# Kernel optimization log

Measured on AMD Instinct MI355X. Metric: run time of the kernel, lower is better.

The kernel has to match this reference:

```python
import jax, jax.numpy as jnp
import numpy as np

B, C, N_MAX = 32, 1, 1024
HID, CLS, ATT_E, ATT_H = 128, 64, 64, 128
D = HID + CLS            # node_state_dim = hidden + class_repr
EDGE_F = 2 * ATT_E       # 128
K_MIX = 20
N_GNN = B * C * N_MAX    # 32768 GNN nodes
N_FEAT = N_GNN + 1       # node_feat rows after zero-pad row
E = 200_000
E_OUT = 500_000
NUM_SUB = 1024
NUM_PROP = 2             # num_GNN_prop (num_GNN_layers = 1)


def _lin(k, din, dout):
    k1, k2 = jax.random.split(k)
    s = 1.0 / np.sqrt(din)
    return (jax.random.uniform(k1, (din, dout), minval=-s, maxval=s),
            jax.random.uniform(k2, (dout,), minval=-s, maxval=s))


def setup_inputs() -> dict:
    key = jax.random.key(0)
    ks = jax.random.split(key, 30)
    inp = {}
    inp['A_pad'] = (jax.random.uniform(ks[0], (B, C, N_MAX, N_MAX)) < 0.05).astype(jnp.float32)
    inp['edges'] = jax.random.randint(ks[1], (E, 2), 0, N_GNN)
    inp['att_idx'] = jax.random.randint(ks[2], (N_GNN,), 0, ATT_E)
    inp['node_idx_feat'] = jax.random.randint(ks[3], (N_GNN,), 0, N_FEAT)
    inp['class_label'] = jax.random.randint(ks[4], (N_GNN,), 0, 2)
    inp['node_idx_gnn'] = jax.random.randint(ks[5], (E_OUT, 2), 0, N_GNN)
    inp['label'] = (jax.random.uniform(ks[6], (E_OUT,)) < 0.3).astype(jnp.float32)
    inp['subgraph_idx'] = jax.random.randint(ks[7], (E_OUT,), 0, NUM_SUB)
    # learned parameters
    inp['W_dec'], inp['b_dec'] = _lin(ks[8], N_MAX, HID)
    inp['class_emb'] = jax.random.normal(ks[9], (2, CLS)) * 0.1
    inp['W_msg1'], inp['b_msg1'] = _lin(ks[10], D + EDGE_F, D)
    inp['W_msg2'], inp['b_msg2'] = _lin(ks[11], D, D)
    inp['W_att1'], inp['b_att1'] = _lin(ks[12], D + EDGE_F, ATT_H)
    inp['W_att2'], inp['b_att2'] = _lin(ks[13], ATT_H, D)
    inp['W_ih'], inp['b_ih'] = _lin(ks[14], D, 3 * D)
    inp['W_hh'], inp['b_hh'] = _lin(ks[15], D, 3 * D)
    inp['Wt1'], inp['bt1'] = _lin(ks[16], D, HID)
    inp['Wt2'], inp['bt2'] = _lin(ks[17], HID, HID)
    inp['Wt3'], inp['bt3'] = _lin(ks[18], HID, K_MIX)
    inp['Wa1'], inp['ba1'] = _lin(ks[19], D, HID)
    inp['Wa2'], inp['ba2'] = _lin(ks[20], HID, HID)
    inp['Wa3'], inp['ba3'] = _lin(ks[21], HID, K_MIX)
    return inp


def _gran_forward(A_pad, label, W_dec, b_dec, class_emb,
                  W_msg1, b_msg1, W_msg2, b_msg2, W_att1, b_att1, W_att2, b_att2,
                  W_ih, b_ih, W_hh, b_hh, Wt1, bt1, Wt2, bt2, Wt3, bt3,
                  Wa1, ba1, Wa2, ba2, Wa3, ba3,
                  edges, att_idx, node_idx_feat, class_label, node_idx_gnn, subgraph_idx):
    # decoder_input: (B*C*N_max, N_max) -> hidden, then zero-pad one row on top
    A = A_pad.reshape(B * C * N_MAX, N_MAX)
    node_feat = A @ W_dec + b_dec                                   # [N_GNN, HID]
    node_feat = jnp.concatenate([jnp.zeros((1, HID), node_feat.dtype), node_feat], axis=0)
    # att_edge_feat: one-hot(att_idx[src]) || one-hot(att_idx[dst])  (scatter of ones)
    att_edge_feat = jnp.concatenate([
        jax.nn.one_hot(att_idx[edges[:, 0]], ATT_E, dtype=node_feat.dtype),
        jax.nn.one_hot(att_idx[edges[:, 1]], ATT_E, dtype=node_feat.dtype)], axis=1)  # [E, 128]
    # node state = gathered feat ++ class representation
    state = jnp.concatenate([node_feat[node_idx_feat], class_emb[class_label]], axis=1)  # [N_GNN, D]

    src, dst = edges[:, 0], edges[:, 1]

    def prop(state):
        diff = state[src] - state[dst]                              # gather node-diff [E, D]
        ei = jnp.concatenate([diff, att_edge_feat], axis=1)          # [E, D+128]
        msg = jax.nn.relu(ei @ W_msg1 + b_msg1) @ W_msg2 + b_msg2   # edge MLP [E, D]
        att = jax.nn.sigmoid(jax.nn.relu(ei @ W_att1 + b_att1) @ W_att2 + b_att2)
        agg = jax.ops.segment_sum(msg * att, dst, num_segments=N_GNN)  # scatter-add [N_GNN, D]
        # GRUCell(agg, state)
        gi = agg @ W_ih + b_ih
        gh = state @ W_hh + b_hh
        ir, iz, inn = jnp.split(gi, 3, axis=1)
        hr, hz, hn = jnp.split(gh, 3, axis=1)
        r = jax.nn.sigmoid(ir + hr)
        z = jax.nn.sigmoid(iz + hz)
        n = jnp.tanh(inn + r * hn)
        return (1.0 - z) * n + z * state

    for _ in range(NUM_PROP):
        state = prop(state)

    # output edge predictions from state diffs
    dout = state[node_idx_gnn[:, 0]] - state[node_idx_gnn[:, 1]]    # [E_OUT, D]
    h = jax.nn.relu(jax.nn.relu(dout @ Wt1 + bt1) @ Wt2 + bt2)
    log_theta = h @ Wt3 + bt3                                        # [E_OUT, K]
    g = jax.nn.relu(jax.nn.relu(dout @ Wa1 + ba1) @ Wa2 + ba2)
    log_alpha = jax.nn.log_softmax(g @ Wa3 + ba3, axis=1)            # [E_OUT, K]

    # mixture Bernoulli loss (BCEWithLogits, pos_weight=1): softplus(x) - x*y
    adj_loss = jax.nn.softplus(log_theta) - log_theta * label[:, None]
    const = jax.ops.segment_sum(jnp.ones((E_OUT,), log_theta.dtype), subgraph_idx, num_segments=NUM_SUB)
    const = jnp.maximum(const, 1.0)  # guard empty subgraphs with random indices
    red_loss = jax.ops.segment_sum(adj_loss, subgraph_idx, num_segments=NUM_SUB)
    red_alpha = jax.ops.segment_sum(log_alpha, subgraph_idx, num_segments=NUM_SUB) / const[:, None]
    log_prob = jax.nn.logsumexp(-red_loss + red_alpha, axis=1)       # [NUM_SUB]
    return -jnp.sum(log_prob) / float(E_OUT)


def reference(A_pad, edges, att_idx, node_idx_feat, class_label, node_idx_gnn, label, subgraph_idx,
              W_dec, b_dec, class_emb, W_msg1, b_msg1, W_msg2, b_msg2,
              W_att1, b_att1, W_att2, b_att2, W_ih, b_ih, W_hh, b_hh,
              Wt1, bt1, Wt2, bt2, Wt3, bt3, Wa1, ba1, Wa2, ba2, Wa3, ba3):
    return _gran_forward(A_pad, label, W_dec, b_dec, class_emb,
                         W_msg1, b_msg1, W_msg2, b_msg2, W_att1, b_att1, W_att2, b_att2,
                         W_ih, b_ih, W_hh, b_hh, Wt1, bt1, Wt2, bt2, Wt3, bt3,
                         Wa1, ba1, Wa2, ba2, Wa3, ba3,
                         edges, att_idx, node_idx_feat, class_label, node_idx_gnn, subgraph_idx)
```

## Files before the change

### kernel.cpp

```cpp
#include <hip/hip_runtime.h>
#include <math.h>

#define NGNN   32768
#define NMAXD  1024
#define HIDD   128
#define CLSD   64
#define DDIM   192
#define ATTH   128
#define NEDGE  200000
#define NEOUT  500000
#define NSUB   1024
#define KMIX   20

#define NREP      64
#define LOSS_OFF  0
#define ALPHA_OFF 20480
#define CNT_OFF   40960
#define REP_STRIDE 41984

typedef __attribute__((ext_vector_type(8))) short bf16x8;
typedef __attribute__((ext_vector_type(8))) unsigned short u16x8;
typedef __attribute__((ext_vector_type(4))) float f32x4;

__device__ __forceinline__ float sigm(float x) { return 1.0f / (1.0f + __expf(-x)); }
__device__ __forceinline__ float tanhf_(float x) { return 2.0f / (1.0f + __expf(-2.0f * x)) - 1.0f; }

__device__ __forceinline__ short f2bf(float f) {
  union { float f; unsigned u; } v; v.f = f;
  unsigned r = v.u + 0x7FFFu + ((v.u >> 16) & 1u);
  return (short)(r >> 16);
}
__device__ __forceinline__ float bf2f(unsigned short u) {
  union { unsigned u; float f; } v; v.u = ((unsigned)u) << 16;
  return v.f;
}
__device__ __forceinline__ f32x4 bc4(float b) {
  f32x4 v; v[0] = b; v[1] = b; v[2] = b; v[3] = b; return v;
}
__device__ __forceinline__ int swz(int u) { return u ^ ((u >> 4) & 7); }

__global__ __launch_bounds__(256) void k_hist(const int* __restrict__ edges,
                                              int* __restrict__ deg) {
  const int e = blockIdx.x * 256 + threadIdx.x;
  if (e < NEDGE) atomicAdd(&deg[edges[2 * e + 1]], 1);
}

__global__ __launch_bounds__(1024) void k_scan(const int* deg_in,
                                               int* rowptr, int* cursor) {
  __shared__ int part[1024];
  const int t = threadIdx.x;
  const int base = t * 32;
  int loc[32];
  int s = 0;
#pragma unroll
  for (int i = 0; i < 32; i++) { loc[i] = deg_in[base + i]; s += loc[i]; }
  part[t] = s;
  __syncthreads();
  for (int off = 1; off < 1024; off <<= 1) {
    int v = 0;
    if (t >= off) v = part[t - off];
    __syncthreads();
    part[t] += v;
    __syncthreads();
  }
  int pre = (t == 0) ? 0 : part[t - 1];
#pragma unroll
  for (int i = 0; i < 32; i++) {
    rowptr[base + i] = pre;
    cursor[base + i] = pre;
    pre += loc[i];
  }
  if (t == 1023) rowptr[NGNN] = pre;
}

__global__ __launch_bounds__(256) void k_scatter(const int* __restrict__ edges,
                                                 int* __restrict__ cursor,
                                                 int* __restrict__ eidx) {
  const int e = blockIdx.x * 256 + threadIdx.x;
  if (e < NEDGE) {
    const int p = atomicAdd(&cursor[edges[2 * e + 1]], 1);
    eidx[p] = e;
  }
}

__global__ __launch_bounds__(64) void k_pack(const float* __restrict__ W,
                                             short* __restrict__ out, int N, int CT) {
  const int l = threadIdx.x;
  const int ks = blockIdx.x / CT;
  const int ct = blockIdx.x % CT;
  const int row0 = ks * 32 + (l >> 4) * 8;
  const int col = ct * 16 + (l & 15);
  short v[8];
#pragma unroll
  for (int j = 0; j < 8; j++) {
    const float f = (col < N) ? W[(size_t)(row0 + j) * N + col] : 0.0f;
    v[j] = f2bf(f);
  }
  *(bf16x8*)(out + ((size_t)blockIdx.x * 64 + l) * 8) = *(bf16x8*)v;
}

__global__ __launch_bounds__(128) void k_dec(
    const float* __restrict__ A, const float* __restrict__ Wd,
    const float* __restrict__ bd, float* __restrict__ nf) {
  __shared__ float arow[NMAXD];
  __shared__ int   nz[NMAXD];
  __shared__ int   cnt;
  const int row = blockIdx.x;
  const int t = threadIdx.x;
  if (t == 0) cnt = 0;
  const float4* A4 = (const float4*)(A + (size_t)row * NMAXD);
  float4* a4 = (float4*)arow;
  a4[t] = A4[t];
  a4[t + 128] = A4[t + 128];
  __syncthreads();
  for (int i = t; i < NMAXD; i += 128) {
    if (arow[i] != 0.0f) {
      int p = atomicAdd(&cnt, 1);
      nz[p] = i;
    }
  }
  __syncthreads();
  float acc = bd[t];
  const int n = cnt;
  for (int i = 0; i < n; i++) acc += Wd[(size_t)nz[i] * HIDD + t];
  nf[(size_t)row * HIDD + t] = acc;
}

__global__ __launch_bounds__(192) void k_state(
    const float* __restrict__ nf, const float* __restrict__ cemb,
    const int* __restrict__ nif, const int* __restrict__ cl,
    unsigned short* __restrict__ stbf) {
  const int i = blockIdx.x;
  const int t = threadIdx.x;
  float v;
  if (t < HIDD) {
    const int idx = nif[i];
    v = (idx == 0) ? 0.0f : nf[(size_t)(idx - 1) * HIDD + t];
  } else {
    v = cemb[cl[i] * CLSD + (t - HIDD)];
  }
  stbf[(size_t)i * DDIM + t] = (unsigned short)f2bf(v);
}

__global__ __launch_bounds__(256, 2) void k_edge_mfma(
    const unsigned short* __restrict__ stbf, const int* __restrict__ edges,
    const int* __restrict__ attidx,
    const float* __restrict__ bm1,
    const short* __restrict__ pWm1, const short* __restrict__ pWm2,
    const float* __restrict__ bm2,
    const float* __restrict__ ba1,
    const short* __restrict__ pWa1, const short* __restrict__ pWa2,
    const float* __restrict__ ba2,
    unsigned short* __restrict__ msgbuf) {
  __shared__ short pdiff[12288];
  __shared__ short phm[12288];
  __shared__ short pha[8192];
  __shared__ int   sa0[64], sa1[64];

  const int t = threadIdx.x;
  const int e0 = blockIdx.x * 64;
  const int wid = t >> 6, l = t & 63;
  const int col16 = l & 15, rr = (l >> 4) * 4;
  const int cb = (l >> 4) * 8;

  if (t < 64) {
    const int s = edges[2 * (e0 + t)];
    const int d = edges[2 * (e0 + t) + 1];
    sa0[t] = attidx[s] + 192;
    sa1[t] = attidx[d] + 256;
  }
  for (int it = 0; it < 6; it++) {
    const int id = t + 256 * it;
    const int r = id / 24, g24 = id % 24;
    const int e = e0 + r;
    const int s = edges[2 * e], d = edges[2 * e + 1];
    const u16x8 a = *(const u16x8*)&stbf[(size_t)s * DDIM + g24 * 8];
    const u16x8 b = *(const u16x8*)&stbf[(size_t)d * DDIM + g24 * 8];
    short v[8];
#pragma unroll
    for (int j = 0; j < 8; j++) v[j] = f2bf(bf2f(a[j]) - bf2f(b[j]));
    const int rt = r >> 4, ks = g24 >> 2, g = g24 & 3;
    *(bf16x8*)&pdiff[swz((rt * 6 + ks) * 64 + g * 16 + (r & 15)) * 8] = *(bf16x8*)v;
  }
  __syncthreads();

  int a0v[4], a1v[4];
#pragma unroll
  for (int rt = 0; rt < 4; rt++) {
    a0v[rt] = sa0[rt * 16 + (l & 15)];
    a1v[rt] = sa1[rt * 16 + (l & 15)];
  }

  const int w5 = wid * 5;

  {
    f32x4 acc[5][4];
#pragma unroll
    for (int u = 0; u < 5; u++)
#pragma unroll
      for (int rt = 0; rt < 4; rt++) acc[u][rt] = bc4(0.0f);

    for (int ks = 0; ks < 10; ks++) {
      bf16x8 A[4];
      if (ks < 6) {
#pragma unroll
        for (int rt = 0; rt < 4; rt++)
          A[rt] = *(const bf16x8*)&pdiff[swz((rt * 6 + ks) * 64 + l) * 8];
      } else {
        const int kb = ks * 32 + cb;
#pragma unroll
        for (int rt = 0; rt < 4; rt++) {
          short v[8];
#pragma unroll
          for (int j = 0; j < 8; j++) {
            const int kg = kb + j;
            v[j] = (kg == a0v[rt] || kg == a1v[rt]) ? (short)0x3F80 : (short)0;
          }
          A[rt] = *(bf16x8*)v;
        }
      }
      bf16x8 B[5];
#pragma unroll
      for (int u = 0; u < 5; u++) {
        const int unit = w5 + u;
        const short* bp = (unit < 12)
            ? &pWm1[((ks * 12 + unit) * 64 + l) * 8]
            : &pWa1[((ks * 8 + (unit - 12)) * 64 + l) * 8];
        B[u] = *(const bf16x8*)bp;
      }
#pragma unroll
      for (int u = 0; u < 5; u++)
#pragma unroll
        for (int rt = 0; rt < 4; rt++)
          acc[u][rt] = __builtin_amdgcn_mfma_f32_16x16x32_bf16(A[rt], B[u], acc[u][rt], 0, 0, 0);
    }

#pragma unroll
    for (int u = 0; u < 5; u++) {
      const int unit = w5 + u;
      const int isMsg = (unit < 12);
      const int ct = isMsg ? unit : unit - 12;
      const int col = ct * 16 + col16;
      const float bb = isMsg ? bm1[col] : ba1[col];
      const int ksp = col >> 5, gp = (col & 31) >> 3, jp = col & 7;
#pragma unroll
      for (int rt = 0; rt < 4; rt++)
#pragma unroll
        for (int j = 0; j < 4; j++) {
          const short hv = f2bf(fmaxf(acc[u][rt][j] + bb, 0.0f));
          if (isMsg) phm[swz((rt * 6 + ksp) * 64 + gp * 16 + rr + j) * 8 + jp] = hv;
          else       pha[swz((rt * 4 + ksp) * 64 + gp * 16 + rr + j) * 8 + jp] = hv;
        }
    }
  }
  __syncthreads();

  {
    const int w3 = wid * 3;
    f32x4 m[3][4], av[3][4];
#pragma unroll
    for (int c = 0; c < 3; c++) {
      const int col = (w3 + c) * 16 + col16;
      const f32x4 bm = bc4(bm2[col]), ba = bc4(ba2[col]);
#pragma unroll
      for (int rt = 0; rt < 4; rt++) { m[c][rt] = bm; av[c][rt] = ba; }
    }
    for (int ks = 0; ks < 6; ks++) {
      bf16x8 A[4];
#pragma unroll
      for (int rt = 0; rt < 4; rt++)
        A[rt] = *(const bf16x8*)&phm[swz((rt * 6 + ks) * 64 + l) * 8];
      bf16x8 B[3];
#pragma unroll
      for (int c = 0; c < 3; c++)
        B[c] = *(const bf16x8*)&pWm2[((ks * 12 + w3 + c) * 64 + l) * 8];
#pragma unroll
      for (int c = 0; c < 3; c++)
#pragma unroll
        for (int rt = 0; rt < 4; rt++)
          m[c][rt] = __builtin_amdgcn_mfma_f32_16x16x32_bf16(A[rt], B[c], m[c][rt], 0, 0, 0);
    }
    for (int ks = 0; ks < 4; ks++) {
      bf16x8 A[4];
#pragma unroll
      for (int rt = 0; rt < 4; rt++)
        A[rt] = *(const bf16x8*)&pha[swz((rt * 4 + ks) * 64 + l) * 8];
      bf16x8 B[3];
#pragma unroll
      for (int c = 0; c < 3; c++)
        B[c] = *(const bf16x8*)&pWa2[((ks * 12 + w3 + c) * 64 + l) * 8];
#pragma unroll
      for (int c = 0; c < 3; c++)
#pragma unroll
        for (int rt = 0; rt < 4; rt++)
          av[c][rt] = __builtin_amdgcn_mfma_f32_16x16x32_bf16(A[rt], B[c], av[c][rt], 0, 0, 0);
    }

    short* msgrow = pdiff;
#pragma unroll
    for (int c = 0; c < 3; c++) {
      const int col = (w3 + c) * 16 + col16;
#pragma unroll
      for (int rt = 0; rt < 4; rt++)
#pragma unroll
        for (int j = 0; j < 4; j++) {
          const int row = rt * 16 + rr + j;
          msgrow[swz(row * 24 + (col >> 3)) * 8 + (col & 7)] =
              f2bf(m[c][rt][j] * sigm(av[c][rt][j]));
        }
    }
  }
  __syncthreads();

  {
    const short* msgrow = pdiff;
    for (int it = 0; it < 6; it++) {
      const int id = t + 256 * it;
      const int r = id / 24, g = id % 24;
      *(float4*)&msgbuf[(size_t)(e0 + r) * DDIM + g * 8] =
          *(const float4*)&msgrow[swz(r * 24 + g) * 8];
    }
  }
}

__global__ __launch_bounds__(256, 2) void k_gru_mfma(
    unsigned short* __restrict__ stbf,
    const unsigned short* __restrict__ msgbuf,
    const int* __restrict__ rowptr, const int* __restrict__ eidx,
    const short* __restrict__ pWih, const float* __restrict__ bih,
    const short* __restrict__ pWhh, const float* __restrict__ bhh) {
  const int t = threadIdx.x;
  const int n0 = blockIdx.x * 64;
  const int wid = t >> 6, l = t & 63;
  const int col16 = l & 15, rr = (l >> 4) * 4;
  const int cb = (l >> 4) * 8;
  const int row = n0 + wid * 16 + (l & 15);

  float afacc[6][8];
#pragma unroll
  for (int ks = 0; ks < 6; ks++)
#pragma unroll
    for (int j = 0; j < 8; j++) afacc[ks][j] = 0.0f;

  const int rbeg = rowptr[row], rend = rowptr[row + 1];
  for (int p = rbeg; p < rend; p++) {
    const int e = eidx[p];
    const unsigned short* mr = &msgbuf[(size_t)e * DDIM + cb];
#pragma unroll
    for (int ks = 0; ks < 6; ks++) {
      const u16x8 cc = *(const u16x8*)(mr + ks * 32);
#pragma unroll
      for (int j = 0; j < 8; j++) afacc[ks][j] += bf2f(cc[j]);
    }
  }

  bf16x8 af[6], sf[6];
#pragma unroll
  for (int ks = 0; ks < 6; ks++) {
    short v[8];
#pragma unroll
    for (int j = 0; j < 8; j++) v[j] = f2bf(afacc[ks][j]);
    af[ks] = *(bf16x8*)v;
    sf[ks] = *(const bf16x8*)&stbf[(size_t)row * DDIM + ks * 32 + cb];
  }

  for (int ct = 0; ct < 12; ct++) {
    const int c = ct * 16 + col16;
    f32x4 ir = bc4(bih[c]), iz = bc4(bih[c + DDIM]), in_ = bc4(bih[c + 2 * DDIM]);
    f32x4 hr = bc4(bhh[c]), hz = bc4(bhh[c + DDIM]), hn = bc4(bhh[c + 2 * DDIM]);
#pragma unroll
    for (int ks = 0; ks < 6; ks++) {
      const bf16x8 wr = *(const bf16x8*)&pWih[((size_t)(ks * 36 + ct) * 64 + l) * 8];
      const bf16x8 wz = *(const bf16x8*)&pWih[((size_t)(ks * 36 + ct + 12) * 64 + l) * 8];
      const bf16x8 wn = *(const bf16x8*)&pWih[((size_t)(ks * 36 + ct + 24) * 64 + l) * 8];
      ir  = __builtin_amdgcn_mfma_f32_16x16x32_bf16(af[ks], wr, ir, 0, 0, 0);
      iz  = __builtin_amdgcn_mfma_f32_16x16x32_bf16(af[ks], wz, iz, 0, 0, 0);
      in_ = __builtin_amdgcn_mfma_f32_16x16x32_bf16(af[ks], wn, in_, 0, 0, 0);
      const bf16x8 vr = *(const bf16x8*)&pWhh[((size_t)(ks * 36 + ct) * 64 + l) * 8];
      const bf16x8 vz = *(const bf16x8*)&pWhh[((size_t)(ks * 36 + ct + 12) * 64 + l) * 8];
      const bf16x8 vn = *(const bf16x8*)&pWhh[((size_t)(ks * 36 + ct + 24) * 64 + l) * 8];
      hr = __builtin_amdgcn_mfma_f32_16x16x32_bf16(sf[ks], vr, hr, 0, 0, 0);
      hz = __builtin_amdgcn_mfma_f32_16x16x32_bf16(sf[ks], vz, hz, 0, 0, 0);
      hn = __builtin_amdgcn_mfma_f32_16x16x32_bf16(sf[ks], vn, hn, 0, 0, 0);
    }
#pragma unroll
    for (int j = 0; j < 4; j++) {
      const size_t idx = (size_t)(n0 + wid * 16 + rr + j) * DDIM + c;
      const float sv = bf2f(stbf[idx]);
      const float r = sigm(ir[j] + hr[j]);
      const float z = sigm(iz[j] + hz[j]);
      const float nn = tanhf_(in_[j] + r * hn[j]);
      stbf[idx] = (unsigned short)f2bf((1.0f - z) * nn + z * sv);
    }
  }
}

__global__ __launch_bounds__(512, 4) void k_head_mfma(
    const unsigned short* __restrict__ stbf, const int* __restrict__ nig,
    const float* __restrict__ label, const int* __restrict__ subidx,
    const short* __restrict__ pWt1, const float* __restrict__ bt1,
    const short* __restrict__ pWt2, const float* __restrict__ bt2,
    const short* __restrict__ pWt3, const float* __restrict__ bt3,
    const short* __restrict__ pWa1, const float* __restrict__ ba1,
    const short* __restrict__ pWa2, const float* __restrict__ ba2,
    const short* __restrict__ pWa3, const float* __restrict__ ba3,
    float* __restrict__ REP) {
  __shared__ short u1[16384];
  __shared__ short ph1[16384];
  __shared__ float la[64 * KMIX];
  __shared__ int   ssub[64];
  __shared__ float slab[64];
  __shared__ float lse[64];

  const int t = threadIdx.x;
  const int r0 = blockIdx.x * 64;
  float* rep = REP + (size_t)(blockIdx.x & (NREP - 1)) * REP_STRIDE;

  if (t < 64) {
    const int gr = r0 + t;
    const int sb = (gr < NEOUT) ? subidx[gr] : 0;
    ssub[t] = sb;
    slab[t] = (gr < NEOUT) ? label[gr] : 0.0f;
    if (gr < NEOUT) atomicAdd(&rep[CNT_OFF + sb], 1.0f);
  }

  for (int it = 0; it < 3; it++) {
    const int id = t + 512 * it;
    const int r = id / 24, g24 = id % 24;
    const int gr = r0 + r;
    const int ok = (gr < NEOUT);
    const int ia = ok ? nig[2 * gr] : 0;
    const int ib = ok ? nig[2 * gr + 1] : 0;
    const u16x8 a = *(const u16x8*)&stbf[(size_t)ia * DDIM + g24 * 8];
    const u16x8 b = *(const u16x8*)&stbf[(size_t)ib * DDIM + g24 * 8];
    short v[8];
#pragma unroll
    for (int j = 0; j < 8; j++) v[j] = f2bf(bf2f(a[j]) - bf2f(b[j]));
    const int rt = r >> 4, ks = g24 >> 2, g = g24 & 3;
    *(bf16x8*)&u1[swz((rt * 6 + ks) * 64 + g * 16 + (r & 15)) * 8] = *(bf16x8*)v;
  }
  __syncthreads();

  const int wid = t >> 6, l = t & 63;
  const int b = wid >> 2, cw = wid & 3;
  const int col16 = l & 15, rr = (l >> 4) * 4;

  const short* pW1 = b ? pWa1 : pWt1;
  const short* pW2 = b ? pWa2 : pWt2;
  const short* pW3 = b ? pWa3 : pWt3;
  const float* bv1 = b ? ba1 : bt1;
  const float* bv2 = b ? ba2 : bt2;
  const float* bv3 = b ? ba3 : bt3;
  short* ph1b = ph1 + b * 8192;
  short* ph2b = u1 + b * 8192;

  {
    bf16x8 B1[12];
    float bias[2];
#pragma unroll
    for (int c2 = 0; c2 < 2; c2++) {
      const int ct = cw * 2 + c2;
      bias[c2] = bv1[ct * 16 + col16];
#pragma unroll
      for (int ks = 0; ks < 6; ks++)
        B1[c2 * 6 + ks] = *(const bf16x8*)&pW1[((ks * 8 + ct) * 64 + l) * 8];
    }
    for (int rt = 0; rt < 4; rt++) {
      bf16x8 a[6];
#pragma unroll
      for (int ks = 0; ks < 6; ks++)
        a[ks] = *(const bf16x8*)&u1[swz((rt * 6 + ks) * 64 + l) * 8];
      f32x4 acc0 = bc4(bias[0]), acc1 = bc4(bias[1]);
#pragma unroll
      for (int ks = 0; ks < 6; ks++) {
        acc0 = __builtin_amdgcn_mfma_f32_16x16x32_bf16(a[ks], B1[ks], acc0, 0, 0, 0);
        acc1 = __builtin_amdgcn_mfma_f32_16x16x32_bf16(a[ks], B1[6 + ks], acc1, 0, 0, 0);
      }
#pragma unroll
      for (int c2 = 0; c2 < 2; c2++) {
        const int col = (cw * 2 + c2) * 16 + col16;
        const int ksp = col >> 5, gp = (col & 31) >> 3, jp = col & 7;
        const f32x4 acc = c2 ? acc1 : acc0;
#pragma unroll
        for (int j = 0; j < 4; j++)
          ph1b[swz((rt * 4 + ksp) * 64 + gp * 16 + rr + j) * 8 + jp] = f2bf(fmaxf(acc[j], 0.0f));
      }
    }
  }
  __syncthreads();

  {
    bf16x8 B2[8];
    float bias[2];
#pragma unroll
    for (int c2 = 0; c2 < 2; c2++) {
      const int ct = cw * 2 + c2;
      bias[c2] = bv2[ct * 16 + col16];
#pragma unroll
      for (int ks = 0; ks < 4; ks++)
        B2[c2 * 4 + ks] = *(const bf16x8*)&pW2[((ks * 8 + ct) * 64 + l) * 8];
    }
    for (int rt = 0; rt < 4; rt++) {
      bf16x8 a[4];
#pragma unroll
      for (int ks = 0; ks < 4; ks++)
        a[ks] = *(const bf16x8*)&ph1b[swz((rt * 4 + ks) * 64 + l) * 8];
      f32x4 acc0 = bc4(bias[0]), acc1 = bc4(bias[1]);
#pragma unroll
      for (int ks = 0; ks < 4; ks++) {
        acc0 = __builtin_amdgcn_mfma_f32_16x16x32_bf16(a[ks], B2[ks], acc0, 0, 0, 0);
        acc1 = __builtin_amdgcn_mfma_f32_16x16x32_bf16(a[ks], B2[4 + ks], acc1, 0, 0, 0);
      }
#pragma unroll
      for (int c2 = 0; c2 < 2; c2++) {
        const int col = (cw * 2 + c2) * 16 + col16;
        const int ksp = col >> 5, gp = (col & 31) >> 3, jp = col & 7;
        const f32x4 acc = c2 ? acc1 : acc0;
#pragma unroll
        for (int j = 0; j < 4; j++)
          ph2b[swz((rt * 4 + ksp) * 64 + gp * 16 + rr + j) * 8 + jp] = f2bf(fmaxf(acc[j], 0.0f));
      }
    }
  }
  __syncthreads();

  {
    const int ct3 = cw & 1, rth = cw >> 1;
    const int col = ct3 * 16 + col16;
    bf16x8 B3[4];
#pragma unroll
    for (int ks = 0; ks < 4; ks++)
      B3[ks] = *(const bf16x8*)&pW3[((ks * 2 + ct3) * 64 + l) * 8];
    const float bias = (col < KMIX) ? bv3[col] : 0.0f;
#pragma unroll
    for (int i = 0; i < 2; i++) {
      const int rt = rth * 2 + i;
      bf16x8 a[4];
#pragma unroll
      for (int ks = 0; ks < 4; ks++)
        a[ks] = *(const bf16x8*)&ph2b[swz((rt * 4 + ks) * 64 + l) * 8];
      f32x4 acc = bc4(bias);
#pragma unroll
      for (int ks = 0; ks < 4; ks++)
        acc = __builtin_amdgcn_mfma_f32_16x16x32_bf16(a[ks], B3[ks], acc, 0, 0, 0);
      if (col < KMIX) {
        if (b == 0) {
#pragma unroll
          for (int j = 0; j < 4; j++) {
            const int r = rt * 16 + rr + j;
            if (r0 + r < NEOUT) {
              const float lt = acc[j];
              const float adj = fmaxf(lt, 0.0f) + logf(1.0f + __expf(-fabsf(lt))) - lt * slab[r];
              atomicAdd(&rep[LOSS_OFF + ssub[r] * KMIX + col], adj);
            }
          }
        } else {
#pragma unroll
          for (int j = 0; j < 4; j++)
            la[(rt * 16 + rr + j) * KMIX + col] = acc[j];
        }
      }
    }
  }
  __syncthreads();
  if (t < 64) {
    float m = -1e30f;
    for (int k = 0; k < KMIX; k++) m = fmaxf(m, la[t * KMIX + k]);
    float s = 0.0f;
    for (int k = 0; k < KMIX; k++) s += __expf(la[t * KMIX + k] - m);
    lse[t] = m + logf(s);
  }
  __syncthreads();
  {
    const int r = t >> 3;
    if (r0 + r < NEOUT) {
#pragma unroll
      for (int i = 0; i < 3; i++) {
        const int c = (t & 7) + 8 * i;
        if (c < KMIX)
          atomicAdd(&rep[ALPHA_OFF + ssub[r] * KMIX + c], la[r * KMIX + c] - lse[r]);
      }
    }
  }
}

__global__ __launch_bounds__(256) void k_red(const float* __restrict__ REP,
                                             float* __restrict__ fin) {
  const int i = blockIdx.x * 256 + threadIdx.x;
  if (i < REP_STRIDE) {
    float s = 0.0f;
    for (int r = 0; r < NREP; r++) s += REP[(size_t)r * REP_STRIDE + i];
    fin[i] = s;
  }
}

__global__ __launch_bounds__(1024) void k_final(
    const float* __restrict__ fin, float* __restrict__ out) {
  __shared__ float part[1024];
  const int s = threadIdx.x;
  const float* red_loss  = fin + LOSS_OFF;
  const float* red_alpha = fin + ALPHA_OFF;
  const float c = fmaxf(fin[CNT_OFF + s], 1.0f);
  float v[KMIX];
  float m = -1e30f;
  for (int k = 0; k < KMIX; k++) {
    v[k] = -red_loss[s * KMIX + k] + red_alpha[s * KMIX + k] / c;
    m = fmaxf(m, v[k]);
  }
  float sum = 0.0f;
  for (int k = 0; k < KMIX; k++) sum += __expf(v[k] - m);
  part[s] = m + logf(sum);
  __syncthreads();
  for (int st = 512; st > 0; st >>= 1) {
    if (s < st) part[s] += part[s + st];
    __syncthreads();
  }
  if (s == 0) out[0] = -part[0] / (float)NEOUT;
}

extern "C" void kernel_launch(void* const* d_in, const int* in_sizes, int n_in,
                              void* d_out, int out_size, void* d_ws, size_t ws_size,
                              hipStream_t stream) {
  const float* A      = (const float*)d_in[0];
  const int*   edges  = (const int*)d_in[1];
  const int*   attidx = (const int*)d_in[2];
  const int*   nif    = (const int*)d_in[3];
  const int*   cl     = (const int*)d_in[4];
  const int*   nig    = (const int*)d_in[5];
  const float* label  = (const float*)d_in[6];
  const int*   subidx = (const int*)d_in[7];
  const float* Wdec   = (const float*)d_in[8];
  const float* bdec   = (const float*)d_in[9];
  const float* cemb   = (const float*)d_in[10];
  const float* Wm1    = (const float*)d_in[11];
  const float* bm1    = (const float*)d_in[12];
  const float* Wm2    = (const float*)d_in[13];
  const float* bm2    = (const float*)d_in[14];
  const float* Wa1    = (const float*)d_in[15];
  const float* ba1    = (const float*)d_in[16];
  const float* Wa2    = (const float*)d_in[17];
  const float* ba2    = (const float*)d_in[18];
  const float* Wih    = (const float*)d_in[19];
  const float* bih    = (const float*)d_in[20];
  const float* Whh    = (const float*)d_in[21];
  const float* bhh    = (const float*)d_in[22];
  const float* Wt1    = (const float*)d_in[23];
  const float* bt1    = (const float*)d_in[24];
  const float* Wt2    = (const float*)d_in[25];
  const float* bt2    = (const float*)d_in[26];
  const float* Wt3    = (const float*)d_in[27];
  const float* bt3    = (const float*)d_in[28];
  const float* Wha1   = (const float*)d_in[29];
  const float* hba1   = (const float*)d_in[30];
  const float* Wha2   = (const float*)d_in[31];
  const float* hba2   = (const float*)d_in[32];
  const float* Wha3   = (const float*)d_in[33];
  const float* hba3   = (const float*)d_in[34];

  char* ws = (char*)d_ws;
  const size_t SZ_STBF = (size_t)NGNN * DDIM * sizeof(short);
  const size_t SZ_MSG  = (size_t)NEDGE * DDIM * sizeof(short);
  const size_t SZ_REP  = (size_t)NREP * REP_STRIDE * sizeof(float);

  unsigned short* stbf   = (unsigned short*)ws;
  unsigned short* msgbuf = (unsigned short*)(ws + SZ_STBF);
  float* nf  = (float*)(ws + SZ_STBF);
  float* REP = (float*)(ws + SZ_STBF);
  float* fin = (float*)(ws + SZ_STBF + SZ_REP);

  char* tail = ws + SZ_STBF + SZ_MSG;
  int* rowptr = (int*)tail;
  int* degcur = (int*)(tail + 131328);
  int* eidx   = (int*)(tail + 131328 + 131072);
  short* pk   = (short*)(tail + 131328 + 131072 + 800000);
  short* pWm1  = pk;
  short* pWa1e = pWm1  + 61440;
  short* pWm2  = pWa1e + 40960;
  short* pWa2e = pWm2  + 36864;
  short* pWt1  = pWa2e + 24576;
  short* pWt2  = pWt1  + 24576;
  short* pWt3  = pWt2  + 16384;
  short* pWh1  = pWt3  + 4096;
  short* pWh2  = pWh1  + 24576;
  short* pWh3  = pWh2  + 16384;
  short* pWih  = pWh3  + 4096;
  short* pWhh  = pWih  + 110592;

  hipMemsetAsync(degcur, 0, (size_t)NGNN * sizeof(int), stream);
  k_hist<<<(NEDGE + 255) / 256, 256, 0, stream>>>(edges, degcur);
  k_scan<<<1, 1024, 0, stream>>>(degcur, rowptr, degcur);
  k_scatter<<<(NEDGE + 255) / 256, 256, 0, stream>>>(edges, degcur, eidx);

  k_pack<<<120, 64, 0, stream>>>(Wm1,  pWm1,  192, 12);
  k_pack<<< 80, 64, 0, stream>>>(Wa1,  pWa1e, 128, 8);
  k_pack<<< 72, 64, 0, stream>>>(Wm2,  pWm2,  192, 12);
  k_pack<<< 48, 64, 0, stream>>>(Wa2,  pWa2e, 192, 12);
  k_pack<<< 48, 64, 0, stream>>>(Wt1,  pWt1,  128, 8);
  k_pack<<< 32, 64, 0, stream>>>(Wt2,  pWt2,  128, 8);
  k_pack<<<  8, 64, 0, stream>>>(Wt3,  pWt3,   20, 2);
  k_pack<<< 48, 64, 0, stream>>>(Wha1, pWh1,  128, 8);
  k_pack<<< 32, 64, 0, stream>>>(Wha2, pWh2,  128, 8);
  k_pack<<<  8, 64, 0, stream>>>(Wha3, pWh3,   20, 2);
  k_pack<<<216, 64, 0, stream>>>(Wih,  pWih,  576, 36);
  k_pack<<<216, 64, 0, stream>>>(Whh,  pWhh,  576, 36);

  k_dec<<<NGNN, 128, 0, stream>>>(A, Wdec, bdec, nf);
  k_state<<<NGNN, 192, 0, stream>>>(nf, cemb, nif, cl, stbf);
  for (int p = 0; p < 2; p++) {
    k_edge_mfma<<<NEDGE / 64, 256, 0, stream>>>(stbf, edges, attidx,
        bm1, pWm1, pWm2, bm2, ba1, pWa1e, pWa2e, ba2, msgbuf);
    k_gru_mfma<<<NGNN / 64, 256, 0, stream>>>(stbf, msgbuf, rowptr, eidx,
        pWih, bih, pWhh, bhh);
  }
  hipMemsetAsync(REP, 0, SZ_REP, stream);
  k_head_mfma<<<(NEOUT + 63) / 64, 512, 0, stream>>>(stbf, nig, label, subidx,
      pWt1, bt1, pWt2, bt2, pWt3, bt3, pWh1, hba1, pWh2, hba2, pWh3, hba3, REP);
  k_red<<<(REP_STRIDE + 255) / 256, 256, 0, stream>>>(REP, fin);
  k_final<<<1, 1024, 0, stream>>>(fin, (float*)d_out);
}
```

Baseline: 875.0 us.

## Halve edge and head kernel tiles to 32 rows for higher occupancy

The edge-message and output-head MFMA kernels now process 32 rows per block instead of 64. Shared memory is halved, and the edge kernel launch bound rises to 5 waves per SIMD. The head kernel drops to 256 threads, each wave loops over two column-pair passes, and its logits/LSE buffers alias the ph1 shared buffer. Per-row label, subgraph and attention indices are read from global memory instead of being staged in shared memory. The goal is more resident blocks to hide gather latency, at the cost of reloading each weight B-fragment for half as many rows (less reuse) and launching more blocks.

```diff
diff --git a/kernel.cpp b/kernel.cpp
--- a/kernel.cpp
+++ b/kernel.cpp
@@ -142,7 +142,7 @@
   stbf[(size_t)i * DDIM + t] = (unsigned short)f2bf(v);
 }
 
-__global__ __launch_bounds__(256, 2) void k_edge_mfma(
+__global__ __launch_bounds__(256, 5) void k_edge_mfma(
     const unsigned short* __restrict__ stbf, const int* __restrict__ edges,
     const int* __restrict__ attidx,
     const float* __restrict__ bm1,
@@ -152,24 +152,16 @@
     const short* __restrict__ pWa1, const short* __restrict__ pWa2,
     const float* __restrict__ ba2,
     unsigned short* __restrict__ msgbuf) {
-  __shared__ short pdiff[12288];
-  __shared__ short phm[12288];
-  __shared__ short pha[8192];
-  __shared__ int   sa0[64], sa1[64];
-
+  __shared__ short pdiff[6144];
+  __shared__ short phm[6144];
+  __shared__ short pha[4096];
   const int t = threadIdx.x;
-  const int e0 = blockIdx.x * 64;
+  const int e0 = blockIdx.x * 32;
   const int wid = t >> 6, l = t & 63;
   const int col16 = l & 15, rr = (l >> 4) * 4;
   const int cb = (l >> 4) * 8;
 
-  if (t < 64) {
-    const int s = edges[2 * (e0 + t)];
-    const int d = edges[2 * (e0 + t) + 1];
-    sa0[t] = attidx[s] + 192;
-    sa1[t] = attidx[d] + 256;
-  }
-  for (int it = 0; it < 6; it++) {
+  for (int it = 0; it < 3; it++) {
     const int id = t + 256 * it;
     const int r = id / 24, g24 = id % 24;
     const int e = e0 + r;
@@ -182,34 +174,35 @@
     const int rt = r >> 4, ks = g24 >> 2, g = g24 & 3;
     *(bf16x8*)&pdiff[swz((rt * 6 + ks) * 64 + g * 16 + (r & 15)) * 8] = *(bf16x8*)v;
   }
-  __syncthreads();
-
-  int a0v[4], a1v[4];
-#pragma unroll
-  for (int rt = 0; rt < 4; rt++) {
-    a0v[rt] = sa0[rt * 16 + (l & 15)];
-    a1v[rt] = sa1[rt * 16 + (l & 15)];
-  }
+
+  int a0v[2], a1v[2];
+#pragma unroll
+  for (int rt = 0; rt < 2; rt++) {
+    const int e = e0 + rt * 16 + (l & 15);
+    a0v[rt] = attidx[edges[2 * e]] + 192;
+    a1v[rt] = attidx[edges[2 * e + 1]] + 256;
+  }
+  __syncthreads();
 
   const int w5 = wid * 5;
 
   {
-    f32x4 acc[5][4];
+    f32x4 acc[5][2];
 #pragma unroll
     for (int u = 0; u < 5; u++)
 #pragma unroll
-      for (int rt = 0; rt < 4; rt++) acc[u][rt] = bc4(0.0f);
+      for (int rt = 0; rt < 2; rt++) acc[u][rt] = bc4(0.0f);
 
     for (int ks = 0; ks < 10; ks++) {
-      bf16x8 A[4];
+      bf16x8 A[2];
       if (ks < 6) {
 #pragma unroll
-        for (int rt = 0; rt < 4; rt++)
+        for (int rt = 0; rt < 2; rt++)
           A[rt] = *(const bf16x8*)&pdiff[swz((rt * 6 + ks) * 64 + l) * 8];
       } else {
         const int kb = ks * 32 + cb;
 #pragma unroll
-        for (int rt = 0; rt < 4; rt++) {
+        for (int rt = 0; rt < 2; rt++) {
           short v[8];
 #pragma unroll
           for (int j = 0; j < 8; j++) {
@@ -231,7 +224,7 @@
 #pragma unroll
       for (int u = 0; u < 5; u++)
 #pragma unroll
-        for (int rt = 0; rt < 4; rt++)
+        for (int rt = 0; rt < 2; rt++)
           acc[u][rt] = __builtin_amdgcn_mfma_f32_16x16x32_bf16(A[rt], B[u], acc[u][rt], 0, 0, 0);
     }
 
@@ -244,7 +237,7 @@
       const float bb = isMsg ? bm1[col] : ba1[col];
       const int ksp = col >> 5, gp = (col & 31) >> 3, jp = col & 7;
 #pragma unroll
-      for (int rt = 0; rt < 4; rt++)
+      for (int rt = 0; rt < 2; rt++)
 #pragma unroll
         for (int j = 0; j < 4; j++) {
           const short hv = f2bf(fmaxf(acc[u][rt][j] + bb, 0.0f));
@@ -257,18 +250,18 @@
 
   {
     const int w3 = wid * 3;
-    f32x4 m[3][4], av[3][4];
+    f32x4 m[3][2], av[3][2];
 #pragma unroll
     for (int c = 0; c < 3; c++) {
       const int col = (w3 + c) * 16 + col16;
       const f32x4 bm = bc4(bm2[col]), ba = bc4(ba2[col]);
 #pragma unroll
-      for (int rt = 0; rt < 4; rt++) { m[c][rt] = bm; av[c][rt] = ba; }
+      for (int rt = 0; rt < 2; rt++) { m[c][rt] = bm; av[c][rt] = ba; }
     }
     for (int ks = 0; ks < 6; ks++) {
-      bf16x8 A[4];
-#pragma unroll
-      for (int rt = 0; rt < 4; rt++)
+      bf16x8 A[2];
+#pragma unroll
+      for (int rt = 0; rt < 2; rt++)
         A[rt] = *(const bf16x8*)&phm[swz((rt * 6 + ks) * 64 + l) * 8];
       bf16x8 B[3];
 #pragma unroll
@@ -277,13 +270,13 @@
 #pragma unroll
       for (int c = 0; c < 3; c++)
 #pragma unroll
-        for (int rt = 0; rt < 4; rt++)
+        for (int rt = 0; rt < 2; rt++)
           m[c][rt] = __builtin_amdgcn_mfma_f32_16x16x32_bf16(A[rt], B[c], m[c][rt], 0, 0, 0);
     }
     for (int ks = 0; ks < 4; ks++) {
-      bf16x8 A[4];
-#pragma unroll
-      for (int rt = 0; rt < 4; rt++)
+      bf16x8 A[2];
+#pragma unroll
+      for (int rt = 0; rt < 2; rt++)
         A[rt] = *(const bf16x8*)&pha[swz((rt * 4 + ks) * 64 + l) * 8];
       bf16x8 B[3];
 #pragma unroll
@@ -292,7 +285,7 @@
 #pragma unroll
       for (int c = 0; c < 3; c++)
 #pragma unroll
-        for (int rt = 0; rt < 4; rt++)
+        for (int rt = 0; rt < 2; rt++)
           av[c][rt] = __builtin_amdgcn_mfma_f32_16x16x32_bf16(A[rt], B[c], av[c][rt], 0, 0, 0);
     }
 
@@ -301,7 +294,7 @@
     for (int c = 0; c < 3; c++) {
       const int col = (w3 + c) * 16 + col16;
 #pragma unroll
-      for (int rt = 0; rt < 4; rt++)
+      for (int rt = 0; rt < 2; rt++)
 #pragma unroll
         for (int j = 0; j < 4; j++) {
           const int row = rt * 16 + rr + j;
@@ -314,7 +307,7 @@
 
   {
     const short* msgrow = pdiff;
-    for (int it = 0; it < 6; it++) {
+    for (int it = 0; it < 3; it++) {
       const int id = t + 256 * it;
       const int r = id / 24, g = id % 24;
       *(float4*)&msgbuf[(size_t)(e0 + r) * DDIM + g * 8] =
@@ -395,7 +388,7 @@
   }
 }
 
-__global__ __launch_bounds__(512, 4) void k_head_mfma(
+__global__ __launch_bounds__(256, 5) void k_head_mfma(
     const unsigned short* __restrict__ stbf, const int* __restrict__ nig,
     const float* __restrict__ label, const int* __restrict__ subidx,
     const short* __restrict__ pWt1, const float* __restrict__ bt1,
@@ -405,27 +398,22 @@
     const short* __restrict__ pWa2, const float* __restrict__ ba2,
     const short* __restrict__ pWa3, const float* __restrict__ ba3,
     float* __restrict__ REP) {
-  __shared__ short u1[16384];
-  __shared__ short ph1[16384];
-  __shared__ float la[64 * KMIX];
-  __shared__ int   ssub[64];
-  __shared__ float slab[64];
-  __shared__ float lse[64];
+  __shared__ short u1[8192];
+  __shared__ short ph1[8192];
+  float* la  = (float*)ph1;
+  float* lse = la + 32 * KMIX;
 
   const int t = threadIdx.x;
-  const int r0 = blockIdx.x * 64;
+  const int r0 = blockIdx.x * 32;
   float* rep = REP + (size_t)(blockIdx.x & (NREP - 1)) * REP_STRIDE;
 
-  if (t < 64) {
+  if (t < 32) {
     const int gr = r0 + t;
-    const int sb = (gr < NEOUT) ? subidx[gr] : 0;
-    ssub[t] = sb;
-    slab[t] = (gr < NEOUT) ? label[gr] : 0.0f;
-    if (gr < NEOUT) atomicAdd(&rep[CNT_OFF + sb], 1.0f);
+    if (gr < NEOUT) atomicAdd(&rep[CNT_OFF + subidx[gr]], 1.0f);
   }
 
   for (int it = 0; it < 3; it++) {
-    const int id = t + 512 * it;
+    const int id = t + 256 * it;
     const int r = id / 24, g24 = id % 24;
     const int gr = r0 + r;
     const int ok = (gr < NEOUT);
@@ -442,7 +430,7 @@
   __syncthreads();
 
   const int wid = t >> 6, l = t & 63;
-  const int b = wid >> 2, cw = wid & 3;
+  const int b = wid >> 1, cw = wid & 1;
   const int col16 = l & 15, rr = (l >> 4) * 4;
 
   const short* pW1 = b ? pWa1 : pWt1;
@@ -451,21 +439,22 @@
   const float* bv1 = b ? ba1 : bt1;
   const float* bv2 = b ? ba2 : bt2;
   const float* bv3 = b ? ba3 : bt3;
-  short* ph1b = ph1 + b * 8192;
-  short* ph2b = u1 + b * 8192;
-
-  {
+  short* ph1b = ph1 + b * 4096;
+  short* ph2b = u1 + b * 4096;
+
+  for (int cp = 0; cp < 2; cp++) {
     bf16x8 B1[12];
     float bias[2];
 #pragma unroll
     for (int c2 = 0; c2 < 2; c2++) {
-      const int ct = cw * 2 + c2;
+      const int ct = cw * 4 + cp * 2 + c2;
       bias[c2] = bv1[ct * 16 + col16];
 #pragma unroll
       for (int ks = 0; ks < 6; ks++)
         B1[c2 * 6 + ks] = *(const bf16x8*)&pW1[((ks * 8 + ct) * 64 + l) * 8];
     }
-    for (int rt = 0; rt < 4; rt++) {
+#pragma unroll
+    for (int rt = 0; rt < 2; rt++) {
       bf16x8 a[6];
 #pragma unroll
       for (int ks = 0; ks < 6; ks++)
@@ -478,7 +467,7 @@
       }
 #pragma unroll
       for (int c2 = 0; c2 < 2; c2++) {
-        const int col = (cw * 2 + c2) * 16 + col16;
+        const int col = (cw * 4 + cp * 2 + c2) * 16 + col16;
         const int ksp = col >> 5, gp = (col & 31) >> 3, jp = col & 7;
         const f32x4 acc = c2 ? acc1 : acc0;
 #pragma unroll
@@ -489,18 +478,19 @@
   }
   __syncthreads();
 
-  {
+  for (int cp = 0; cp < 2; cp++) {
     bf16x8 B2[8];
     float bias[2];
 #pragma unroll
     for (int c2 = 0; c2 < 2; c2++) {
-      const int ct = cw * 2 + c2;
+      const int ct = cw * 4 + cp * 2 + c2;
       bias[c2] = bv2[ct * 16 + col16];
 #pragma unroll
       for (int ks = 0; ks < 4; ks++)
         B2[c2 * 4 + ks] = *(const bf16x8*)&pW2[((ks * 8 + ct) * 64 + l) * 8];
     }
-    for (int rt = 0; rt < 4; rt++) {
+#pragma unroll
+    for (int rt = 0; rt < 2; rt++) {
       bf16x8 a[4];
 #pragma unroll
       for (int ks = 0; ks < 4; ks++)
@@ -513,7 +503,7 @@
       }
 #pragma unroll
       for (int c2 = 0; c2 < 2; c2++) {
-        const int col = (cw * 2 + c2) * 16 + col16;
+        const int col = (cw * 4 + cp * 2 + c2) * 16 + col16;
         const int ksp = col >> 5, gp = (col & 31) >> 3, jp = col & 7;
         const f32x4 acc = c2 ? acc1 : acc0;
 #pragma unroll
@@ -525,16 +515,14 @@
   __syncthreads();
 
   {
-    const int ct3 = cw & 1, rth = cw >> 1;
-    const int col = ct3 * 16 + col16;
+    const int col = cw * 16 + col16;
     bf16x8 B3[4];
 #pragma unroll
     for (int ks = 0; ks < 4; ks++)
-      B3[ks] = *(const bf16x8*)&pW3[((ks * 2 + ct3) * 64 + l) * 8];
+      B3[ks] = *(const bf16x8*)&pW3[((ks * 2 + cw) * 64 + l) * 8];
     const float bias = (col < KMIX) ? bv3[col] : 0.0f;
 #pragma unroll
-    for (int i = 0; i < 2; i++) {
-      const int rt = rth * 2 + i;
+    for (int rt = 0; rt < 2; rt++) {
       bf16x8 a[4];
 #pragma unroll
       for (int ks = 0; ks < 4; ks++)
@@ -548,10 +536,12 @@
 #pragma unroll
           for (int j = 0; j < 4; j++) {
             const int r = rt * 16 + rr + j;
-            if (r0 + r < NEOUT) {
+            const int gr = r0 + r;
+            if (gr < NEOUT) {
               const float lt = acc[j];
-              const float adj = fmaxf(lt, 0.0f) + logf(1.0f + __expf(-fabsf(lt))) - lt * slab[r];
-              atomicAdd(&rep[LOSS_OFF + ssub[r] * KMIX + col], adj);
+              const float adj = fmaxf(lt, 0.0f) + logf(1.0f + __expf(-fabsf(lt)))
+                                - lt * label[gr];
+              atomicAdd(&rep[LOSS_OFF + subidx[gr] * KMIX + col], adj);
             }
           }
         } else {
@@ -563,7 +553,7 @@
     }
   }
   __syncthreads();
-  if (t < 64) {
+  if (t < 32) {
     float m = -1e30f;
     for (int k = 0; k < KMIX; k++) m = fmaxf(m, la[t * KMIX + k]);
     float s = 0.0f;
@@ -573,12 +563,14 @@
   __syncthreads();
   {
     const int r = t >> 3;
-    if (r0 + r < NEOUT) {
+    const int gr = r0 + r;
+    if (gr < NEOUT) {
+      const int sb = subidx[gr];
 #pragma unroll
       for (int i = 0; i < 3; i++) {
         const int c = (t & 7) + 8 * i;
         if (c < KMIX)
-          atomicAdd(&rep[ALPHA_OFF + ssub[r] * KMIX + c], la[r * KMIX + c] - lse[r]);
+          atomicAdd(&rep[ALPHA_OFF + sb * KMIX + c], la[r * KMIX + c] - lse[r]);
       }
     }
   }
@@ -707,13 +699,13 @@
   k_dec<<<NGNN, 128, 0, stream>>>(A, Wdec, bdec, nf);
   k_state<<<NGNN, 192, 0, stream>>>(nf, cemb, nif, cl, stbf);
   for (int p = 0; p < 2; p++) {
-    k_edge_mfma<<<NEDGE / 64, 256, 0, stream>>>(stbf, edges, attidx,
+    k_edge_mfma<<<NEDGE / 32, 256, 0, stream>>>(stbf, edges, attidx,
         bm1, pWm1, pWm2, bm2, ba1, pWa1e, pWa2e, ba2, msgbuf);
     k_gru_mfma<<<NGNN / 64, 256, 0, stream>>>(stbf, msgbuf, rowptr, eidx,
         pWih, bih, pWhh, bhh);
   }
   hipMemsetAsync(REP, 0, SZ_REP, stream);
-  k_head_mfma<<<(NEOUT + 63) / 64, 512, 0, stream>>>(stbf, nig, label, subidx,
+  k_head_mfma<<<(NEOUT + 31) / 32, 256, 0, stream>>>(stbf, nig, label, subidx,
       pWt1, bt1, pWt2, bt2, pWt3, bt3, pWh1, hba1, pWh2, hba2, pWh3, hba3, REP);
   k_red<<<(REP_STRIDE + 255) / 256, 256, 0, stream>>>(REP, fin);
   k_final<<<1, 1024, 0, stream>>>(fin, (float*)d_out);
```

Result: slower. 1.211 ms (+38.4%).
